# Kernel tuning notes

Measured on AMD Instinct MI355X. Metric: run time of the kernel, lower is better.

The kernel has to match this reference:

```python
import jax, jax.numpy as jnp
import numpy as np

FEAT_RES = 512
FEAT_DIM = 48
WIDTH = 128
IN_DIM = FEAT_DIM + 27 + 63  # 138
N_RAYS, N_SAMPLES = 4096, 128


def positional_encode(x, L):
    freqs = (2.0 ** jnp.arange(L)).astype(x.dtype)            # [L]
    xf = x[..., None, :] * freqs[:, None]                      # [..., L, 3]
    enc = jnp.concatenate([jnp.sin(xf), jnp.cos(xf)], axis=-1) # [..., L, 6]
    return jnp.concatenate([x, enc.reshape(x.shape[:-1] + (L * 6,))], axis=-1)


def grid_sample_bilinear(plane, gx, gy):
    # plane: [C, H, W]; gx, gy: [N, S] in [-1, 1]; align_corners=True, zeros padding
    H, W = plane.shape[-2], plane.shape[-1]
    ix = (gx + 1.0) * 0.5 * (W - 1)
    iy = (gy + 1.0) * 0.5 * (H - 1)
    x0 = jnp.floor(ix); y0 = jnp.floor(iy)
    x1 = x0 + 1.0;      y1 = y0 + 1.0
    wx1 = ix - x0; wx0 = 1.0 - wx1
    wy1 = iy - y0; wy0 = 1.0 - wy1

    def gather(xi, yi, w):
        valid = (xi >= 0) & (xi <= W - 1) & (yi >= 0) & (yi <= H - 1)
        xc = jnp.clip(xi, 0, W - 1).astype(jnp.int32)
        yc = jnp.clip(yi, 0, H - 1).astype(jnp.int32)
        v = plane[:, yc, xc]                                   # [C, N, S]
        return v * (w * valid.astype(w.dtype))[None]

    return (gather(x0, y0, wx0 * wy0) + gather(x1, y0, wx1 * wy0)
            + gather(x0, y1, wx0 * wy1) + gather(x1, y1, wx1 * wy1))


def setup_inputs() -> dict:
    key = jax.random.key(0)
    ks = jax.random.split(key, 12)
    x = jax.random.uniform(ks[0], (N_RAYS, N_SAMPLES, 3), jnp.float32, -3.0, 3.0)
    d = jax.random.normal(ks[1], (N_RAYS, 3), jnp.float32)
    d = d / jnp.linalg.norm(d, axis=-1, keepdims=True)
    feat = jax.random.normal(ks[2], (3, FEAT_DIM, FEAT_RES, FEAT_RES), jnp.float32)
    s = 0.05
    W0 = jax.random.normal(ks[3], (IN_DIM, WIDTH), jnp.float32) * s
    b0 = jnp.zeros((WIDTH,), jnp.float32)
    W1 = jax.random.normal(ks[4], (WIDTH, WIDTH), jnp.float32) * s
    b1 = jnp.zeros((WIDTH,), jnp.float32)
    W2 = jax.random.normal(ks[5], (WIDTH, WIDTH), jnp.float32) * s
    b2 = jnp.zeros((WIDTH,), jnp.float32)
    W3 = jax.random.normal(ks[6], (WIDTH, 4), jnp.float32) * s
    b3 = jnp.zeros((4,), jnp.float32)
    return {"x": x, "d": d, "feat": feat, "W0": W0, "b0": b0,
            "W1": W1, "b1": b1, "W2": W2, "b2": b2, "W3": W3, "b3": b3}


def reference(x, d, feat, W0, b0, W1, b1, W2, b2, W3, b3):
    x = x / 3.0                                                # [N, S, 3]
    f_xy = grid_sample_bilinear(feat[0], x[..., 0], x[..., 1])  # [C, N, S]
    f_yz = grid_sample_bilinear(feat[1], x[..., 1], x[..., 2])
    f_xz = grid_sample_bilinear(feat[2], x[..., 0], x[..., 2])
    f_sum = jnp.moveaxis(f_xy + f_yz + f_xz, 0, -1)            # [N, S, C]

    d_rep = jnp.broadcast_to(d[:, None, :], x.shape)           # [N, S, 3]
    h = jnp.concatenate([f_sum, positional_encode(d_rep, 4), positional_encode(x, 10)], axis=-1)

    h = jax.nn.relu(h @ W0 + b0)
    h = jax.nn.relu(h @ W1 + b1)
    h = jax.nn.relu(h @ W2 + b2)
    out = h @ W3 + b3                                          # [N, S, 4]
    return jnp.concatenate([out[..., :3], jax.nn.relu(out[..., 3:])], axis=-1)
```

## Files before the change

### kernel.cpp

```cpp
#include <hip/hip_runtime.h>
#include <hip/hip_bf16.h>
#include <hip/hip_fp16.h>
#include <cstdint>
#include <cstddef>

#define NPLANE 262144
#define HSTR 144
#define PW_LAYER 18432
#define NCELL 32768
#define NSAMP 524288
#define NRAY 4096

#define WS_FEAT_OFF 131072
#define FEAT_BYTES  75497472
#define WS_CNT_OFF  (WS_FEAT_OFF + FEAT_BYTES)
#define WS_OFFS_OFF (WS_CNT_OFF + 131072)
#define WS_XS_OFF   (WS_OFFS_OFF + 131072)
#define WS_PED_OFF  (WS_XS_OFF + (size_t)NSAMP*16)
#define WS_END      (WS_PED_OFF + (size_t)NRAY*28*2)

#define TRS_BLKS 3072
#define PREP_BLKS 216
#define PED_BLKS 16
#define SCAT_BLKS 2048
#define K2_BLKS (TRS_BLKS + PREP_BLKS + PED_BLKS + SCAT_BLKS)

typedef unsigned int uint;
typedef __attribute__((ext_vector_type(16))) float f32x16;
typedef _Float16 half8 __attribute__((ext_vector_type(8)));

__device__ __forceinline__ unsigned short f16u(float f){
    __half h = __float2half(f);
    return *reinterpret_cast<unsigned short*>(&h);
}
__device__ __forceinline__ f32x16 mfma16_(half8 a, half8 b, f32x16 c){
    return __builtin_amdgcn_mfma_f32_32x32x16_f16(a, b, c, 0,0,0);
}

__device__ __forceinline__ uint part3(uint v){
    v &= 0x3ff;
    v = (v | (v<<16)) & 0x030000FFu;
    v = (v | (v<<8))  & 0x0300F00Fu;
    v = (v | (v<<4))  & 0x030C30C3u;
    v = (v | (v<<2))  & 0x09249249u;
    return v;
}
__device__ __forceinline__ uint cellkey(float x0, float x1, float x2){
    const float s = 1.0f/3.0f;
    const int cx = min(max((int)((x0*s+1.0f)*16.0f),0),31);
    const int cy = min(max((int)((x1*s+1.0f)*16.0f),0),31);
    const int cz = min(max((int)((x2*s+1.0f)*16.0f),0),31);
    return part3((uint)cx) | (part3((uint)cy)<<1) | (part3((uint)cz)<<2);
}

__global__ __launch_bounds__(256) void hist_k(const float* __restrict__ x, uint* __restrict__ counts){
    const int i = blockIdx.x*256 + threadIdx.x;
    if (i >= NSAMP) return;
    atomicAdd(&counts[cellkey(x[3*i], x[3*i+1], x[3*i+2])], 1u);
}

__global__ __launch_bounds__(1024) void scan_k(const uint* __restrict__ counts, uint* __restrict__ offs){
    __shared__ uint ps[1024];
    const int t = threadIdx.x;
    uint loc[32]; uint s = 0;
    #pragma unroll
    for (int i=0;i<32;++i){ loc[i] = counts[t*32+i]; s += loc[i]; }
    ps[t] = s; __syncthreads();
    for (int off=1; off<1024; off<<=1){
        uint v = (t>=off) ? ps[t-off] : 0u;
        __syncthreads();
        ps[t] += v;
        __syncthreads();
    }
    uint base = ps[t] - s;
    #pragma unroll
    for (int i=0;i<32;++i){ offs[t*32+i] = base; base += loc[i]; }
}

__global__ __launch_bounds__(256) void prepass_k(const float* __restrict__ feat,
                                                 const float* __restrict__ W0,
                                                 const float* __restrict__ W1,
                                                 const float* __restrict__ W2,
                                                 const float* __restrict__ b0,
                                                 const float* __restrict__ b1,
                                                 const float* __restrict__ b2,
                                                 const float* __restrict__ d,
                                                 const float* __restrict__ x,
                                                 uint* __restrict__ offs,
                                                 unsigned short* __restrict__ featT,
                                                 unsigned short* __restrict__ wp,
                                                 unsigned short* __restrict__ ped,
                                                 float4* __restrict__ xs){
    const int bid = blockIdx.x, tid = threadIdx.x;
    if (bid < TRS_BLKS){
        __shared__ unsigned short lb[256*50];
        const int pos = bid*256 + tid;
        const int p  = pos >> 18;
        const int yx = pos & (NPLANE-1);
        const float* src = feat + (size_t)p*48*NPLANE + yx;
        #pragma unroll 4
        for (int c = 0; c < 48; ++c){
            lb[tid*50 + c] = f16u(src[(size_t)c*NPLANE]);
        }
        __syncthreads();
        uint4* dst = (uint4*)(featT + (size_t)bid*(256*48));
        #pragma unroll
        for (int m = 0; m < 6; ++m){
            const int u4 = tid + m*256;
            const int byteoff = u4*16;
            const int smp = byteoff/96;
            const int off = (byteoff%96) >> 2;
            const uint* rw = (const uint*)(lb + smp*50);
            uint4 val; val.x = rw[off]; val.y = rw[off+1]; val.z = rw[off+2]; val.w = rw[off+3];
            dst[u4] = val;
        }
        return;
    }
    if (bid < TRS_BLKS + PREP_BLKS){
        const int idx = (bid - TRS_BLKS)*256 + tid;
        if (idx >= 3*PW_LAYER) return;
        const int L = idx / PW_LAYER, base = idx % PW_LAYER;
        const float* W = (L==0)? W0 : (L==1)? W1 : W2;
        const float* B = (L==0)? b0 : (L==1)? b1 : b2;
        const int KREAL = (L==0)? 138 : 128;
        const int e  = base & 7;
        const int l  = (base >> 3) & 63;
        const int fr = base >> 9;
        const int ks = fr >> 2, nt = fr & 3;
        const int k  = ks*16 + (l >> 5)*8 + e;
        const int n  = nt*32 + (l & 31);
        float v = 0.f;
        if (k < KREAL) v = W[k*128 + n];
        else if (k == KREAL) v = B[n];
        wp[idx] = f16u(v);
        return;
    }
    if (bid < TRS_BLKS + PREP_BLKS + PED_BLKS){
        const int ray = (bid - TRS_BLKS - PREP_BLKS)*256 + tid;
        if (ray >= NRAY) return;
        const float dv0 = d[ray*3], dv1 = d[ray*3+1], dv2 = d[ray*3+2];
        unsigned short* row = ped + ray*28;
        row[0]=f16u(dv0); row[1]=f16u(dv1); row[2]=f16u(dv2);
        #pragma unroll
        for (int l=0;l<4;++l){
            const float sc = (float)(1<<l);
            float sv, cv;
            __sincosf(dv0*sc, &sv, &cv); row[3+l*6+0]=f16u(sv); row[3+l*6+3]=f16u(cv);
            __sincosf(dv1*sc, &sv, &cv); row[3+l*6+1]=f16u(sv); row[3+l*6+4]=f16u(cv);
            __sincosf(dv2*sc, &sv, &cv); row[3+l*6+2]=f16u(sv); row[3+l*6+5]=f16u(cv);
        }
        row[27] = 0;
        return;
    }
    {
        const int i = (bid - TRS_BLKS - PREP_BLKS - PED_BLKS)*256 + tid;
        if (i >= NSAMP) return;
        const float x0 = x[3*i], x1 = x[3*i+1], x2 = x[3*i+2];
        const uint pos = atomicAdd(&offs[cellkey(x0,x1,x2)], 1u);
        xs[pos] = make_float4(x0, x1, x2, __int_as_float(i));
    }
}

__device__ __forceinline__ void run_layer_ns(unsigned short* H, const unsigned short* __restrict__ Wp,
                                             int lane, int ln31, int kg, int wid, const int* pr){
    const unsigned short* Hrow0 = H + ln31*HSTR;
    const unsigned short* Hrow1 = H + (32+ln31)*HSTR;
    const int ntb = 2*wid;
    f32x16 acc00=(f32x16)0.f, acc01=(f32x16)0.f, acc10=(f32x16)0.f, acc11=(f32x16)0.f;
    {
        half8 bf[10];
        #pragma unroll
        for (int i=0;i<10;++i){
            const int ks = i>>1, nt = ntb + (i&1);
            bf[i] = *reinterpret_cast<const half8*>(Wp + (((ks*4+nt)*64 + lane) << 3));
        }
        #pragma unroll
        for (int ks=0; ks<5; ++ks){
            const half8 a0 = *reinterpret_cast<const half8*>(Hrow0 + ks*16 + kg*8);
            const half8 a1 = *reinterpret_cast<const half8*>(Hrow1 + ks*16 + kg*8);
            acc00 = mfma16_(a0, bf[2*ks],   acc00);
            acc01 = mfma16_(a0, bf[2*ks+1], acc01);
            acc10 = mfma16_(a1, bf[2*ks],   acc10);
            acc11 = mfma16_(a1, bf[2*ks+1], acc11);
        }
    }
    {
        half8 bf[8];
        #pragma unroll
        for (int i=0;i<8;++i){
            const int ks = 5 + (i>>1), nt = ntb + (i&1);
            bf[i] = *reinterpret_cast<const half8*>(Wp + (((ks*4+nt)*64 + lane) << 3));
        }
        #pragma unroll
        for (int ks=5; ks<9; ++ks){
            const half8 a0 = *reinterpret_cast<const half8*>(Hrow0 + ks*16 + kg*8);
            const half8 a1 = *reinterpret_cast<const half8*>(Hrow1 + ks*16 + kg*8);
            acc00 = mfma16_(a0, bf[2*(ks-5)],   acc00);
            acc01 = mfma16_(a0, bf[2*(ks-5)+1], acc01);
            acc10 = mfma16_(a1, bf[2*(ks-5)],   acc10);
            acc11 = mfma16_(a1, bf[2*(ks-5)+1], acc11);
        }
    }
    __syncthreads();
    #pragma unroll
    for (int r=0;r<16;++r){
        const int row = pr[r] >> 8;
        const int col = ntb*32 + (pr[r] & 255);
        H[row*HSTR + col]           = f16u(fmaxf(acc00[r], 0.f));
        H[row*HSTR + col + 32]      = f16u(fmaxf(acc01[r], 0.f));
        H[(row+32)*HSTR + col]      = f16u(fmaxf(acc10[r], 0.f));
        H[(row+32)*HSTR + col + 32] = f16u(fmaxf(acc11[r], 0.f));
    }
    __syncthreads();
}

__global__ __launch_bounds__(128, 4) void nerf_mfma(
    const unsigned short* __restrict__ featT,
    const unsigned short* __restrict__ wp0, const unsigned short* __restrict__ wp1,
    const unsigned short* __restrict__ wp2,
    const float* __restrict__ W3, const float* __restrict__ b3,
    const float4* __restrict__ xs, const unsigned short* __restrict__ ped,
    float* __restrict__ out)
{
    __shared__ unsigned short H[64*HSTR];
    __shared__ uint sW3u[256];
    __shared__ float4 sX[64];

    const int tid  = threadIdx.x;
    const int wid  = tid >> 6, lane = tid & 63;
    const int ln31 = lane & 31, kg = lane >> 5;
    const int sbase = wid * 32;
    const int base = (((int)blockIdx.x & 7)*1024 + ((int)blockIdx.x >> 3))*64 + sbase;
    unsigned short* Hw = H + sbase*HSTR;

    half8 pa = (half8)0, pb = (half8)0, qa = (half8)0, qb = (half8)0;
    if (kg == 0){
        pa[0] = (_Float16)(float)ln31;
        pb[0] = (_Float16)1.0f;
        qa[0] = (_Float16)1.0f;
        qb[0] = (_Float16)(float)ln31;
    }
    const f32x16 zz = (f32x16)0.f;
    const f32x16 D1 = mfma16_(pa, pb, zz);
    const f32x16 D2 = mfma16_(qa, qb, zz);
    int pr[16];
    #pragma unroll
    for (int r=0;r<16;++r) pr[r] = (((int)D1[r]) << 8) | (int)D2[r];

    if (lane < 32) sX[sbase + lane] = xs[base + lane];
    #pragma unroll
    for (int j=0;j<2;++j){
        const int idx = lane*2 + j;
        const int i2 = wid*128 + idx;
        const int k = i2 >> 1, c = i2 & 1;
        sW3u[i2] = ((uint)f16u(W3[k*4 + 2*c])) | (((uint)f16u(W3[k*4 + 2*c + 1])) << 16);
    }

    #pragma unroll
    for (int rr=0; rr<2; ++rr){
        if (rr == 1 && lane >= 32) break;
        const int s32 = rr ? lane : ln31;
        const int m   = rr ? 2 : kg;
        const float4 xr = sX[sbase + s32];
        const float xn = ((m==0)? xr.x : (m==1)? xr.y : xr.z) * (1.0f/3.0f);
        unsigned short* row = H + (sbase+s32)*HSTR;
        row[75+m] = f16u(xn);
        float sv, cv;
        __sincosf(xn, &sv, &cv);
        #pragma unroll
        for (int l=0;l<10;++l){
            row[78+l*6+m]   = f16u(sv);
            row[78+l*6+3+m] = f16u(cv);
            const float s2v = 2.0f*sv*cv;
            const float c2v = 1.0f - 2.0f*sv*sv;
            sv = s2v; cv = c2v;
        }
    }

    {
        const int s32 = lane >> 1, hf = lane & 1;
        const int sid = __float_as_int(sX[sbase + s32].w);
        const uint* src = (const uint*)(ped + (sid >> 7)*28) + hf*7;
        uint* dstu = (uint*)(H + (sbase+s32)*HSTR + 48) + hf*7;
        if (hf == 0){
            #pragma unroll
            for (int i=0;i<7;++i) dstu[i] = src[i];
        } else {
            #pragma unroll
            for (int i=0;i<6;++i) dstu[i] = src[i];
            H[(sbase+s32)*HSTR + 74] = ((const unsigned short*)src)[12];
        }
    }

    if (lane < 32){
        *(uint*)(H + (sbase+lane)*HSTR + 138)  = 0x00003C00u;
        *(uint2*)(H + (sbase+lane)*HSTR + 140) = make_uint2(0u, 0u);
    }

    #pragma unroll
    for (int rr=0; rr<3; ++rr){
        const int u = rr*64 + lane;
        const int s32 = u/6, ch = u - s32*6;
        const float4 xr = sX[sbase + s32];
        const float xn0 = xr.x*(1.0f/3.0f);
        const float xn1 = xr.y*(1.0f/3.0f);
        const float xn2 = xr.z*(1.0f/3.0f);
        const int c0 = ch*8;
        __half2 acc[4];
        #pragma unroll
        for (int q=0;q<4;++q) acc[q] = __float2half2_rn(0.f);
        #pragma unroll
        for (int p=0;p<3;++p){
            const float gx = (p==1)? xn1 : xn0;
            const float gy = (p==0)? xn1 : xn2;
            const float ix = ((gx+1.0f)*0.5f)*511.0f;
            const float iy = ((gy+1.0f)*0.5f)*511.0f;
            const float fx0 = floorf(ix), fy0 = floorf(iy);
            const float wx1 = ix - fx0, wy1 = iy - fy0;
            const float wx0 = 1.0f-wx1, wy0 = 1.0f-wy1;
            const int x0i = (int)fx0, y0i = (int)fy0;
            const int x0c = min(max(x0i,0),511),   x1c = min(max(x0i+1,0),511);
            const int y0c = min(max(y0i,0),511),   y1c = min(max(y0i+1,0),511);
            const uint r0 = (uint)(p*NPLANE + y0c*512);
            const uint r1 = (uint)(p*NPLANE + y1c*512);
            const uint  av[4] = {(r0+x0c)*48u, (r0+x1c)*48u, (r1+x0c)*48u, (r1+x1c)*48u};
            const float wv[4] = {wx0*wy0, wx1*wy0, wx0*wy1, wx1*wy1};
            #pragma unroll
            for (int cr=0;cr<4;++cr){
                const uint4 uv = *(const uint4*)(featT + av[cr] + c0);
                const __half2 w2 = __float2half2_rn(wv[cr]);
                union { uint4 v; __half2 h[4]; } t; t.v = uv;
                acc[0] = __hfma2(t.h[0], w2, acc[0]);
                acc[1] = __hfma2(t.h[1], w2, acc[1]);
                acc[2] = __hfma2(t.h[2], w2, acc[2]);
                acc[3] = __hfma2(t.h[3], w2, acc[3]);
            }
        }
        union { __half2 h[4]; uint4 v; } pk;
        #pragma unroll
        for (int q=0;q<4;++q) pk.h[q] = acc[q];
        *(uint4*)(H + (sbase+s32)*HSTR + c0) = pk.v;
    }
    __syncthreads();

    run_layer_ns(H, wp0, lane, ln31, kg, wid, pr);
    {
        const int row = tid & 63, hf = tid >> 6;
        if (hf == 0) *(uint4*)(H + row*HSTR + 128) = make_uint4(0x00003C00u,0u,0u,0u);
        else         *(uint4*)(H + row*HSTR + 136) = make_uint4(0u,0u,0u,0u);
    }
    __syncthreads();
    run_layer_ns(H, wp1, lane, ln31, kg, wid, pr);
    run_layer_ns(H, wp2, lane, ln31, kg, wid, pr);

    {
        const int s32 = lane >> 1, cp = lane & 1;
        const unsigned short* hrow = Hw + s32*HSTR;
        const int sid = __float_as_int(sX[sbase + s32].w);
        const int jp = 2*cp;
        const float2 b3v = *(const float2*)(b3 + jp);
        float a0 = b3v.x, a1 = b3v.y;
        #pragma unroll
        for (int q=0;q<16;++q){
            union { uint4 v; __half2 h[4]; } u;
            u.v = *(const uint4*)(hrow + q*8);
            const int k = q*8;
            #pragma unroll
            for (int j2=0;j2<4;++j2){
                const float2 f = __half22float2(u.h[j2]);
                const int k2 = k + j2*2;
                union { uint u32; __half2 h; } w0c, w1c;
                w0c.u32 = sW3u[(k2+0)*2+cp];
                w1c.u32 = sW3u[(k2+1)*2+cp];
                const float2 w0f = __half22float2(w0c.h);
                const float2 w1f = __half22float2(w1c.h);
                a0 += f.x*w0f.x + f.y*w1f.x;
                a1 += f.x*w0f.y + f.y*w1f.y;
            }
        }
        if (cp == 1) a1 = fmaxf(a1, 0.f);
        float2 o; o.x = a0; o.y = a1;
        *(float2*)(out + (size_t)sid*4 + jp) = o;
    }
}

#define STR 148
#define SBLK 64
template<int K4, int KTAIL>
__device__ __forceinline__ void mlp_layer_fb(float (*Hs)[STR], const float* __restrict__ W,
                                             const float* __restrict__ B, int tid){
    const int tx = tid & 31, ty = tid >> 5;
    const int s0 = ty*8, j0 = tx*4;
    float acc[8][4];
    #pragma unroll
    for (int i=0;i<8;++i){ acc[i][0]=0.f; acc[i][1]=0.f; acc[i][2]=0.f; acc[i][3]=0.f; }
    for (int kk = 0; kk < K4; ++kk){
        const int k = kk*4;
        const float4 wa = *(const float4*)(W + (size_t)(k+0)*128 + j0);
        const float4 wb = *(const float4*)(W + (size_t)(k+1)*128 + j0);
        const float4 wc = *(const float4*)(W + (size_t)(k+2)*128 + j0);
        const float4 wd = *(const float4*)(W + (size_t)(k+3)*128 + j0);
        #pragma unroll
        for (int i=0;i<8;++i){
            const float4 h = *(const float4*)&Hs[s0+i][k];
            acc[i][0] += h.x*wa.x + h.y*wb.x + h.z*wc.x + h.w*wd.x;
            acc[i][1] += h.x*wa.y + h.y*wb.y + h.z*wc.y + h.w*wd.y;
            acc[i][2] += h.x*wa.z + h.y*wb.z + h.z*wc.z + h.w*wd.z;
            acc[i][3] += h.x*wa.w + h.y*wb.w + h.z*wc.w + h.w*wd.w;
        }
    }
    #pragma unroll
    for (int t=0;t<KTAIL;++t){
        const int k = K4*4+t;
        const float4 wa = *(const float4*)(W + (size_t)k*128 + j0);
        #pragma unroll
        for (int i=0;i<8;++i){
            const float h = Hs[s0+i][k];
            acc[i][0] += h*wa.x; acc[i][1] += h*wa.y; acc[i][2] += h*wa.z; acc[i][3] += h*wa.w;
        }
    }
    const float4 bb = *(const float4*)(B + j0);
    __syncthreads();
    #pragma unroll
    for (int i=0;i<8;++i){
        float4 o;
        o.x = fmaxf(acc[i][0]+bb.x, 0.f);
        o.y = fmaxf(acc[i][1]+bb.y, 0.f);
        o.z = fmaxf(acc[i][2]+bb.z, 0.f);
        o.w = fmaxf(acc[i][3]+bb.w, 0.f);
        *(float4*)&Hs[s0+i][j0] = o;
    }
    __syncthreads();
}

__global__ __launch_bounds__(256) void nerf_fused_fb(
    const float* __restrict__ x, const float* __restrict__ d,
    const float* __restrict__ feat,
    const float* __restrict__ W0, const float* __restrict__ b0,
    const float* __restrict__ W1, const float* __restrict__ b1,
    const float* __restrict__ W2, const float* __restrict__ b2,
    const float* __restrict__ W3, const float* __restrict__ b3,
    float* __restrict__ out)
{
    __shared__ float Hs[SBLK][STR];
    __shared__ uint4  sA[3][SBLK];
    __shared__ float4 sW[3][SBLK];

    const int tid = threadIdx.x;
    const int g0 = blockIdx.x * SBLK;

    if (tid < 192){
        const int s = tid & 63, p = tid >> 6;
        const int g = g0 + s;
        const float xn0 = x[3*g+0]/3.0f, xn1 = x[3*g+1]/3.0f, xn2 = x[3*g+2]/3.0f;
        const float gx = (p==1)? xn1 : xn0;
        const float gy = (p==0)? xn1 : xn2;
        const float ix = ((gx+1.0f)*0.5f)*511.0f;
        const float iy = ((gy+1.0f)*0.5f)*511.0f;
        const float fx0 = floorf(ix), fy0 = floorf(iy);
        const float wx1 = ix - fx0, wy1 = iy - fy0;
        const float wx0 = 1.0f-wx1, wy0 = 1.0f-wy1;
        const int x0i = (int)fx0, y0i = (int)fy0;
        const int x0c = min(max(x0i,0),511),   x1c = min(max(x0i+1,0),511);
        const int y0c = min(max(y0i,0),511),   y1c = min(max(y0i+1,0),511);
        const uint bp = (uint)p*48u*NPLANE;
        sA[p][s] = make_uint4(bp + y0c*512 + x0c, bp + y0c*512 + x1c,
                              bp + y1c*512 + x0c, bp + y1c*512 + x1c);
        sW[p][s] = make_float4(wx0*wy0, wx1*wy0, wx0*wy1, wx1*wy1);
    }
    if (tid < 64){
        const int s = tid, g = g0 + s;
        float xn[3];
        xn[0]=x[3*g+0]/3.0f; xn[1]=x[3*g+1]/3.0f; xn[2]=x[3*g+2]/3.0f;
        Hs[s][75]=xn[0]; Hs[s][76]=xn[1]; Hs[s][77]=xn[2];
        float f = 1.0f;
        for (int l=0;l<10;++l){
            #pragma unroll
            for (int m=0;m<3;++m){
                const float a = xn[m]*f;
                Hs[s][78+l*6+m]   = sinf(a);
                Hs[s][78+l*6+3+m] = cosf(a);
            }
            f *= 2.0f;
        }
    } else if (tid < 91){
        const int k = tid-64;
        const int ray = g0 >> 7;
        float v;
        if (k < 3) v = d[ray*3+k];
        else {
            const int l=(k-3)/6, r=(k-3)%6;
            const float a = d[ray*3 + (r%3)] * (float)(1<<l);
            v = (r<3)? sinf(a) : cosf(a);
        }
        for (int s2=0;s2<64;++s2) Hs[s2][48+k]=v;
    }
    __syncthreads();

    for (int it = tid; it < 384; it += 256){
        const int s = it & 63;
        const int c0 = (it >> 6)*8;
        float acc[8];
        #pragma unroll
        for (int q=0;q<8;++q) acc[q]=0.f;
        #pragma unroll
        for (int p=0;p<3;++p){
            const uint4  aa = sA[p][s];
            const float4 ww = sW[p][s];
            const uint  av[4] = {aa.x,aa.y,aa.z,aa.w};
            const float wv[4] = {ww.x,ww.y,ww.z,ww.w};
            #pragma unroll
            for (int cr=0;cr<4;++cr){
                const float w = wv[cr];
                const float* bsrc = feat + av[cr] + (size_t)c0*NPLANE;
                #pragma unroll
                for (int q=0;q<8;++q) acc[q] += w*bsrc[(size_t)q*NPLANE];
            }
        }
        *(float4*)&Hs[s][c0]   = make_float4(acc[0],acc[1],acc[2],acc[3]);
        *(float4*)&Hs[s][c0+4] = make_float4(acc[4],acc[5],acc[6],acc[7]);
    }
    __syncthreads();

    mlp_layer_fb<34,2>(Hs, W0, b0, tid);
    mlp_layer_fb<32,0>(Hs, W1, b1, tid);
    mlp_layer_fb<32,0>(Hs, W2, b2, tid);

    {
        const int s = tid>>2, j = tid&3;
        float acc = 0.f;
        for (int kk=0; kk<32; ++kk){
            const float4 h = *(const float4*)&Hs[s][kk*4];
            const int k = kk*4;
            acc += h.x*W3[(k+0)*4+j] + h.y*W3[(k+1)*4+j]
                 + h.z*W3[(k+2)*4+j] + h.w*W3[(k+3)*4+j];
        }
        acc += b3[j];
        if (j==3) acc = fmaxf(acc, 0.f);
        out[(size_t)blockIdx.x*256 + tid] = acc;
    }
}

extern "C" void kernel_launch(void* const* d_in, const int* in_sizes, int n_in,
                              void* d_out, int out_size, void* d_ws, size_t ws_size,
                              hipStream_t stream){
    (void)in_sizes; (void)n_in; (void)out_size;
    const float* x    = (const float*)d_in[0];
    const float* ddir = (const float*)d_in[1];
    const float* feat = (const float*)d_in[2];
    const float* W0 = (const float*)d_in[3];  const float* b0 = (const float*)d_in[4];
    const float* W1 = (const float*)d_in[5];  const float* b1 = (const float*)d_in[6];
    const float* W2 = (const float*)d_in[7];  const float* b2 = (const float*)d_in[8];
    const float* W3 = (const float*)d_in[9];  const float* b3 = (const float*)d_in[10];
    float* out = (float*)d_out;

    char* wsb = (char*)d_ws;

    if (ws_size >= WS_END){
        unsigned short* wsu   = (unsigned short*)wsb;
        unsigned short* featT = (unsigned short*)(wsb + WS_FEAT_OFF);
        uint*   counts = (uint*)(wsb + WS_CNT_OFF);
        uint*   offs   = (uint*)(wsb + WS_OFFS_OFF);
        float4* xsrec  = (float4*)(wsb + WS_XS_OFF);
        unsigned short* ped = (unsigned short*)(wsb + WS_PED_OFF);
        hipMemsetAsync(counts, 0, NCELL*sizeof(uint), stream);
        hist_k<<<2048, 256, 0, stream>>>(x, counts);
        scan_k<<<1, 1024, 0, stream>>>(counts, offs);
        prepass_k<<<K2_BLKS, 256, 0, stream>>>(feat, W0, W1, W2, b0, b1, b2, ddir, x,
                                               offs, featT, wsu, ped, xsrec);
        nerf_mfma<<<8192, 128, 0, stream>>>(featT,
                                            wsu, wsu + PW_LAYER, wsu + 2*PW_LAYER,
                                            W3, b3, xsrec, ped, out);
    } else {
        nerf_fused_fb<<<8192, 256, 0, stream>>>(x, ddir, feat,
                                                W0,b0,W1,b1,W2,b2,W3,b3, out);
    }
}
```

Before: 255.4 us.

## Split MLP layers across four waves with 256-thread blocks

Blocks grow from two to four waves for the same 64 samples. Each wave now computes one 32-column N-tile for all 64 rows, with two accumulators instead of four. Setup work (encoding, feature gather, output) is spread over all 256 threads with added block barriers. The aim is fewer weight-fragment registers per wave and more waves in flight to hide gather and MFMA latency, at the cost of more synchronization and idle threads in some phases.

```diff
diff --git a/kernel.cpp b/kernel.cpp
--- a/kernel.cpp
+++ b/kernel.cpp
@@ -161,60 +161,49 @@
     }
 }
 
-__device__ __forceinline__ void run_layer_ns(unsigned short* H, const unsigned short* __restrict__ Wp,
-                                             int lane, int ln31, int kg, int wid, const int* pr){
+__device__ __forceinline__ void run_layer_ns4(unsigned short* H, const unsigned short* __restrict__ Wp,
+                                              int lane, int ln31, int kg, int wid, const int* pr){
     const unsigned short* Hrow0 = H + ln31*HSTR;
     const unsigned short* Hrow1 = H + (32+ln31)*HSTR;
-    const int ntb = 2*wid;
-    f32x16 acc00=(f32x16)0.f, acc01=(f32x16)0.f, acc10=(f32x16)0.f, acc11=(f32x16)0.f;
+    f32x16 acc0=(f32x16)0.f, acc1=(f32x16)0.f;
     {
-        half8 bf[10];
-        #pragma unroll
-        for (int i=0;i<10;++i){
-            const int ks = i>>1, nt = ntb + (i&1);
-            bf[i] = *reinterpret_cast<const half8*>(Wp + (((ks*4+nt)*64 + lane) << 3));
-        }
+        half8 bf[5];
+        #pragma unroll
+        for (int i=0;i<5;++i)
+            bf[i] = *reinterpret_cast<const half8*>(Wp + (((i*4+wid)*64 + lane) << 3));
         #pragma unroll
         for (int ks=0; ks<5; ++ks){
             const half8 a0 = *reinterpret_cast<const half8*>(Hrow0 + ks*16 + kg*8);
             const half8 a1 = *reinterpret_cast<const half8*>(Hrow1 + ks*16 + kg*8);
-            acc00 = mfma16_(a0, bf[2*ks],   acc00);
-            acc01 = mfma16_(a0, bf[2*ks+1], acc01);
-            acc10 = mfma16_(a1, bf[2*ks],   acc10);
-            acc11 = mfma16_(a1, bf[2*ks+1], acc11);
+            acc0 = mfma16_(a0, bf[ks], acc0);
+            acc1 = mfma16_(a1, bf[ks], acc1);
         }
     }
     {
-        half8 bf[8];
-        #pragma unroll
-        for (int i=0;i<8;++i){
-            const int ks = 5 + (i>>1), nt = ntb + (i&1);
-            bf[i] = *reinterpret_cast<const half8*>(Wp + (((ks*4+nt)*64 + lane) << 3));
-        }
+        half8 bf[4];
+        #pragma unroll
+        for (int i=0;i<4;++i)
+            bf[i] = *reinterpret_cast<const half8*>(Wp + ((((5+i)*4+wid)*64 + lane) << 3));
         #pragma unroll
         for (int ks=5; ks<9; ++ks){
             const half8 a0 = *reinterpret_cast<const half8*>(Hrow0 + ks*16 + kg*8);
             const half8 a1 = *reinterpret_cast<const half8*>(Hrow1 + ks*16 + kg*8);
-            acc00 = mfma16_(a0, bf[2*(ks-5)],   acc00);
-            acc01 = mfma16_(a0, bf[2*(ks-5)+1], acc01);
-            acc10 = mfma16_(a1, bf[2*(ks-5)],   acc10);
-            acc11 = mfma16_(a1, bf[2*(ks-5)+1], acc11);
+            acc0 = mfma16_(a0, bf[ks-5], acc0);
+            acc1 = mfma16_(a1, bf[ks-5], acc1);
         }
     }
     __syncthreads();
     #pragma unroll
     for (int r=0;r<16;++r){
         const int row = pr[r] >> 8;
-        const int col = ntb*32 + (pr[r] & 255);
-        H[row*HSTR + col]           = f16u(fmaxf(acc00[r], 0.f));
-        H[row*HSTR + col + 32]      = f16u(fmaxf(acc01[r], 0.f));
-        H[(row+32)*HSTR + col]      = f16u(fmaxf(acc10[r], 0.f));
-        H[(row+32)*HSTR + col + 32] = f16u(fmaxf(acc11[r], 0.f));
-    }
-    __syncthreads();
-}
-
-__global__ __launch_bounds__(128, 4) void nerf_mfma(
+        const int col = wid*32 + (pr[r] & 255);
+        H[row*HSTR + col]      = f16u(fmaxf(acc0[r], 0.f));
+        H[(row+32)*HSTR + col] = f16u(fmaxf(acc1[r], 0.f));
+    }
+    __syncthreads();
+}
+
+__global__ __launch_bounds__(256, 5) void nerf_mfma(
     const unsigned short* __restrict__ featT,
     const unsigned short* __restrict__ wp0, const unsigned short* __restrict__ wp1,
     const unsigned short* __restrict__ wp2,
@@ -229,9 +218,7 @@
     const int tid  = threadIdx.x;
     const int wid  = tid >> 6, lane = tid & 63;
     const int ln31 = lane & 31, kg = lane >> 5;
-    const int sbase = wid * 32;
-    const int base = (((int)blockIdx.x & 7)*1024 + ((int)blockIdx.x >> 3))*64 + sbase;
-    unsigned short* Hw = H + sbase*HSTR;
+    const int gbase = (((int)blockIdx.x & 7)*1024 + ((int)blockIdx.x >> 3))*64;
 
     half8 pa = (half8)0, pb = (half8)0, qa = (half8)0, qb = (half8)0;
     if (kg == 0){
@@ -247,23 +234,18 @@
     #pragma unroll
     for (int r=0;r<16;++r) pr[r] = (((int)D1[r]) << 8) | (int)D2[r];
 
-    if (lane < 32) sX[sbase + lane] = xs[base + lane];
-    #pragma unroll
-    for (int j=0;j<2;++j){
-        const int idx = lane*2 + j;
-        const int i2 = wid*128 + idx;
-        const int k = i2 >> 1, c = i2 & 1;
-        sW3u[i2] = ((uint)f16u(W3[k*4 + 2*c])) | (((uint)f16u(W3[k*4 + 2*c + 1])) << 16);
-    }
-
-    #pragma unroll
-    for (int rr=0; rr<2; ++rr){
-        if (rr == 1 && lane >= 32) break;
-        const int s32 = rr ? lane : ln31;
-        const int m   = rr ? 2 : kg;
-        const float4 xr = sX[sbase + s32];
+    if (tid < 64) sX[tid] = xs[gbase + tid];
+    {
+        const int k = tid >> 1, c = tid & 1;
+        sW3u[tid] = ((uint)f16u(W3[k*4 + 2*c])) | (((uint)f16u(W3[k*4 + 2*c + 1])) << 16);
+    }
+    __syncthreads();
+
+    if (tid < 192){
+        const int s32 = tid & 63, m = tid >> 6;
+        const float4 xr = sX[s32];
         const float xn = ((m==0)? xr.x : (m==1)? xr.y : xr.z) * (1.0f/3.0f);
-        unsigned short* row = H + (sbase+s32)*HSTR;
+        unsigned short* row = H + s32*HSTR;
         row[75+m] = f16u(xn);
         float sv, cv;
         __sincosf(xn, &sv, &cv);
@@ -277,31 +259,32 @@
         }
     }
 
-    {
-        const int s32 = lane >> 1, hf = lane & 1;
-        const int sid = __float_as_int(sX[sbase + s32].w);
+    if (tid < 128){
+        const int s32 = tid >> 1, hf = tid & 1;
+        const int sid = __float_as_int(sX[s32].w);
         const uint* src = (const uint*)(ped + (sid >> 7)*28) + hf*7;
-        uint* dstu = (uint*)(H + (sbase+s32)*HSTR + 48) + hf*7;
+        uint* dstu = (uint*)(H + s32*HSTR + 48) + hf*7;
         if (hf == 0){
             #pragma unroll
             for (int i=0;i<7;++i) dstu[i] = src[i];
         } else {
             #pragma unroll
             for (int i=0;i<6;++i) dstu[i] = src[i];
-            H[(sbase+s32)*HSTR + 74] = ((const unsigned short*)src)[12];
-        }
-    }
-
-    if (lane < 32){
-        *(uint*)(H + (sbase+lane)*HSTR + 138)  = 0x00003C00u;
-        *(uint2*)(H + (sbase+lane)*HSTR + 140) = make_uint2(0u, 0u);
-    }
-
-    #pragma unroll
-    for (int rr=0; rr<3; ++rr){
-        const int u = rr*64 + lane;
+            H[s32*HSTR + 74] = ((const unsigned short*)src)[12];
+        }
+    }
+
+    if (tid < 64){
+        *(uint*)(H + tid*HSTR + 138)  = 0x00003C00u;
+        *(uint2*)(H + tid*HSTR + 140) = make_uint2(0u, 0u);
+    }
+
+    #pragma unroll
+    for (int rr=0; rr<2; ++rr){
+        const int u = rr*256 + tid;
+        if (rr == 1 && tid >= 128) break;
         const int s32 = u/6, ch = u - s32*6;
-        const float4 xr = sX[sbase + s32];
+        const float4 xr = sX[s32];
         const float xn0 = xr.x*(1.0f/3.0f);
         const float xn1 = xr.y*(1.0f/3.0f);
         const float xn2 = xr.z*(1.0f/3.0f);
@@ -339,24 +322,24 @@
         union { __half2 h[4]; uint4 v; } pk;
         #pragma unroll
         for (int q=0;q<4;++q) pk.h[q] = acc[q];
-        *(uint4*)(H + (sbase+s32)*HSTR + c0) = pk.v;
-    }
-    __syncthreads();
-
-    run_layer_ns(H, wp0, lane, ln31, kg, wid, pr);
-    {
+        *(uint4*)(H + s32*HSTR + c0) = pk.v;
+    }
+    __syncthreads();
+
+    run_layer_ns4(H, wp0, lane, ln31, kg, wid, pr);
+    if (tid < 128){
         const int row = tid & 63, hf = tid >> 6;
         if (hf == 0) *(uint4*)(H + row*HSTR + 128) = make_uint4(0x00003C00u,0u,0u,0u);
         else         *(uint4*)(H + row*HSTR + 136) = make_uint4(0u,0u,0u,0u);
     }
     __syncthreads();
-    run_layer_ns(H, wp1, lane, ln31, kg, wid, pr);
-    run_layer_ns(H, wp2, lane, ln31, kg, wid, pr);
-
-    {
-        const int s32 = lane >> 1, cp = lane & 1;
-        const unsigned short* hrow = Hw + s32*HSTR;
-        const int sid = __float_as_int(sX[sbase + s32].w);
+    run_layer_ns4(H, wp1, lane, ln31, kg, wid, pr);
+    run_layer_ns4(H, wp2, lane, ln31, kg, wid, pr);
+
+    if (tid < 128){
+        const int s32 = tid >> 1, cp = tid & 1;
+        const unsigned short* hrow = H + s32*HSTR;
+        const int sid = __float_as_int(sX[s32].w);
         const int jp = 2*cp;
         const float2 b3v = *(const float2*)(b3 + jp);
         float a0 = b3v.x, a1 = b3v.y;
@@ -568,7 +551,7 @@
         scan_k<<<1, 1024, 0, stream>>>(counts, offs);
         prepass_k<<<K2_BLKS, 256, 0, stream>>>(feat, W0, W1, W2, b0, b1, b2, ddir, x,
                                                offs, featT, wsu, ped, xsrec);
-        nerf_mfma<<<8192, 128, 0, stream>>>(featT,
+        nerf_mfma<<<8192, 256, 0, stream>>>(featT,
                                             wsu, wsu + PW_LAYER, wsu + 2*PW_LAYER,
                                             W3, b3, xsrec, ped, out);
     } else {
```

After: 241.9 us, median of 2. 5.3% less time.
